# Kernel optimization log

Measured on AMD Instinct MI355X. Metric: run time of the kernel, lower is better.

## Reference

```python
import jax, jax.numpy as jnp
import numpy as np

DX = 1.0
DZ_MIN = 1.0
K = 3  # median filter kernel size (odd)


def median_filter3d(x):
    # x: (N, C, D, H, W); 3x3x3 windowed median with reflect padding.
    p = K // 2
    xp = jnp.pad(x, ((0, 0), (0, 0), (p, p), (p, p), (p, p)), mode='reflect')
    N, C, D, H, W = x.shape
    # 27 shifted views stacked on a new last axis (fixed small loop over kernel offsets)
    wins = jnp.stack(
        [xp[:, :, i:i + D, j:j + H, k:k + W]
         for i in range(K) for j in range(K) for k in range(K)],
        axis=-1,
    )
    # 27 elements (odd) -> torch lower-median == element at index 13 of sorted window
    return jnp.sort(wins, axis=-1)[..., (K * K * K - 1) // 2]


def setup_inputs() -> dict:
    key = jax.random.key(0)
    pred_z = jax.random.normal(key, (1, 1, 128, 192, 193), dtype=jnp.float32)
    return {"pred_z": pred_z, "iepoch": 1, "epoch_max": 100}


def reference(pred_z, iepoch, epoch_max):
    # dz along last (W) axis
    dz = pred_z[..., 1:] - pred_z[..., :-1]
    d = dz / DX
    # windowed-median smoothness loss (no NaNs in inputs -> nanmean == mean)
    smoothz = median_filter3d(d)
    loss_smooth = jnp.mean((d - smoothz) ** 2)
    # monotonicity penalty: max over clamped negative increments
    loss_mon = jnp.max(jnp.maximum(-(dz - DZ_MIN) / DX, 0.0))
    # torch.median over all elements returns sorted[(n-1)//2] (lower median)
    z0 = pred_z[..., 0].reshape(-1)
    n = z0.shape[0]
    loss_average = jnp.sort(z0)[(n - 1) // 2] ** 2
    return (loss_smooth, loss_mon, loss_average)
```

## Files before the change

### kernel.cpp

```cpp
#include <hip/hip_runtime.h>

#define NZ 128
#define NY 192
#define NXP 193
#define NX 192
#define NVOX (NZ * NY * NX)
#define NZ0 (NZ * NY)

#define TX 32
#define TY 16
#define TZ 8
#define LX 34
#define LYP 10
#define LZ 10
#define LSLP (LYP * LX)
#define LTOTP (LZ * LSLP)

#define GX (NX / TX)
#define GY (NY / TY)
#define GZ (NZ / TZ)
#define NBLK (GX * GY * GZ)
#define ZB (NZ0 / 256)

__device__ double   g_ps[NBLK];
__device__ float    g_pm[NBLK];
__device__ unsigned g_hist[2048];
__device__ unsigned g_u[NZ0];

__device__ __forceinline__ int refl(int i, int n) {
    i = (i < 0) ? -i : i;
    i = (i >= n) ? (2 * n - 2 - i) : i;
    return i;
}

__device__ __forceinline__ unsigned f2sortable(float f) {
    unsigned bits = __float_as_uint(f);
    return bits ^ ((bits & 0x80000000u) ? 0xFFFFFFFFu : 0x80000000u);
}

typedef _Float16 H2 __attribute__((ext_vector_type(2)));

static __device__ __forceinline__ H2 h2min(H2 a, H2 b) { return __builtin_elementwise_min(a, b); }
static __device__ __forceinline__ H2 h2max(H2 a, H2 b) { return __builtin_elementwise_max(a, b); }

template<int M, int N>
struct OEM {
    static __device__ __forceinline__ void run(const H2* a, const H2* b, H2* out) {
        if constexpr (M == 0) {
#pragma unroll
            for (int i = 0; i < N; ++i) out[i] = b[i];
        } else if constexpr (N == 0) {
#pragma unroll
            for (int i = 0; i < M; ++i) out[i] = a[i];
        } else if constexpr (M == 1 && N == 1) {
            out[0] = h2min(a[0], b[0]);
            out[1] = h2max(a[0], b[0]);
        } else {
            constexpr int ME = (M + 1) / 2, MO = M / 2, NE = (N + 1) / 2, NO = N / 2;
            H2 ae[ME], be[NE];
            H2 ao[MO > 0 ? MO : 1], bo[NO > 0 ? NO : 1];
#pragma unroll
            for (int i = 0; i < ME; ++i) ae[i] = a[2 * i];
#pragma unroll
            for (int i = 0; i < MO; ++i) ao[i] = a[2 * i + 1];
#pragma unroll
            for (int i = 0; i < NE; ++i) be[i] = b[2 * i];
#pragma unroll
            for (int i = 0; i < NO; ++i) bo[i] = b[2 * i + 1];
            constexpr int EL = ME + NE, OL = MO + NO;
            H2 e[EL];
            H2 o[OL > 0 ? OL : 1];
            OEM<ME, NE>::run(ae, be, e);
            OEM<MO, NO>::run(ao, bo, o);
            constexpr int P = (OL < EL - 1) ? OL : (EL - 1);
            out[0] = e[0];
#pragma unroll
            for (int i = 0; i < P; ++i) {
                out[2 * i + 1] = h2min(o[i], e[i + 1]);
                out[2 * i + 2] = h2max(o[i], e[i + 1]);
            }
            if constexpr (EL == OL)           out[M + N - 1] = o[OL - 1];
            else if constexpr (EL == OL + 2)  out[M + N - 1] = e[EL - 1];
        }
    }
};

template<int N>
struct OES {
    static __device__ __forceinline__ void run(const H2* in, H2* out) {
        if constexpr (N == 1) {
            out[0] = in[0];
        } else {
            constexpr int H = N / 2;
            H2 s1[H], s2[N - H];
            OES<H>::run(in, s1);
            OES<N - H>::run(in + H, s2);
            OEM<H, N - H>::run(s1, s2, out);
        }
    }
};

__device__ __forceinline__ H2 sel27(const H2* A, const H2* M) {
    H2 t0 = h2max(A[0], M[12]);
    H2 t1 = h2max(A[1], M[11]);
    H2 t2 = h2max(A[2], M[10]);
    H2 t3 = h2max(A[3], M[9]);
    H2 t4 = h2max(A[4], M[8]);
    H2 t5 = h2max(A[5], M[7]);
    H2 t6 = h2max(A[6], M[6]);
    H2 t7 = h2max(A[7], M[5]);
    H2 t8 = h2max(A[8], M[4]);
    H2 r0 = h2min(h2min(t0, t1), h2min(t2, t3));
    H2 r1 = h2min(h2min(t4, t5), h2min(t6, t7));
    return h2min(h2min(r0, r1), h2min(t8, M[13]));
}

__global__ __launch_bounds__(256, 4) void fused_main(const float* __restrict__ P) {
    __shared__ H2 dt[LTOTP];
    const int tid = threadIdx.x;
    const int bid = blockIdx.x;

    if (bid < ZB) {
        unsigned* h = (unsigned*)dt;
        for (int j = tid; j < 2048; j += 256) h[j] = 0u;
        __syncthreads();
        const int i = bid * 256 + tid;
        unsigned u = f2sortable(P[(size_t)i * NXP]);
        g_u[i] = u;
        atomicAdd(&h[u >> 21], 1u);
        __syncthreads();
        for (int j = tid; j < 2048; j += 256) {
            unsigned c = h[j];
            if (c) atomicAdd(&g_hist[j], c);
        }
        return;
    }

    const int bf = bid - ZB;
    const int bx = bf % GX;
    const int brem = bf / GX;
    const int by = brem % GY;
    const int bz = brem / GY;
    const int x0 = bx * TX, y0 = by * TY, z0t = bz * TZ;

    int offL[2], offH[2], lp[2];
#pragma unroll
    for (int k = 0; k < 2; ++k) {
        int p = tid + 256 * k;
        lp[k] = (p < LSLP) ? p : -1;
        if (p < LSLP) {
            int xx = p % LX, rr = p / LX;
            int gx  = refl(x0 + xx - 1, NX);
            int gyL = refl(y0 + rr - 1, NY);
            int gyH = refl(y0 + rr + 7, NY);
            offL[k] = gyL * NXP + gx;
            offH[k] = gyH * NXP + gx;
        }
    }
    for (int zz = 0; zz < LZ; ++zz) {
        int gz = refl(z0t + zz - 1, NZ);
        const float* __restrict__ pl = P + (size_t)gz * (NY * NXP);
#pragma unroll
        for (int k = 0; k < 2; ++k) {
            if (lp[k] >= 0) {
                float dL = pl[offL[k] + 1] - pl[offL[k]];
                float dH = pl[offH[k] + 1] - pl[offH[k]];
                H2 v;
                v.x = (_Float16)dL;
                v.y = (_Float16)dH;
                dt[zz * LSLP + lp[k]] = v;
            }
        }
    }
    __syncthreads();

    const int x = tid & 31;
    const int y = tid >> 5;
    const int rbase = y * LX + x;

    auto rd9 = [&](int base, H2* v) {
#pragma unroll
        for (int dy = 0; dy < 3; ++dy)
#pragma unroll
            for (int dxx = 0; dxx < 3; ++dxx)
                v[dy * 3 + dxx] = dt[base + dy * LX + dxx];
    };

    H2 S0[9], S1[9], S2[9], T[9], M[18];
    H2 c2, m2 = (H2)((_Float16)0.0f);
    const H2 one2 = (H2)((_Float16)1.0f);
    float s_acc = 0.0f;

    rd9(rbase, T);            OES<9>::run(T, S0);
    rd9(rbase + LSLP, T);     c2 = T[4];
    OES<9>::run(T, S1);

    auto accum = [&](H2 med) {
        H2 df = c2 - med;
        float dl = (float)df.x, dh = (float)df.y;
        s_acc = fmaf(dl, dl, fmaf(dh, dh, s_acc));
        m2 = h2max(m2, one2 - c2);
    };

    int sl = rbase + 2 * LSLP;
#pragma unroll 1
    for (int t = 0; t < TZ; t += 2) {
        rd9(sl, T);
        H2 cn = T[4];
        OES<9>::run(T, S2);
        OEM<9, 9>::run(S1, S2, M);
        accum(sel27(S0, M));
        c2 = cn;
        sl += LSLP;

        rd9(sl, T);
        cn = T[4];
        OES<9>::run(T, S0);
        accum(sel27(S0, M));
        c2 = cn;
        sl += LSLP;

#pragma unroll
        for (int i = 0; i < 9; ++i) {
            H2 tmp = S0[i];
            S0[i] = S2[i];
            S1[i] = tmp;
        }
    }

    float m_acc = fmaxf((float)m2.x, (float)m2.y);

#pragma unroll
    for (int off = 32; off > 0; off >>= 1) {
        s_acc += __shfl_down(s_acc, off);
        m_acc = fmaxf(m_acc, __shfl_down(m_acc, off));
    }
    __shared__ float ss[4], sm[4];
    const int lane = tid & 63, wid = tid >> 6;
    if (lane == 0) { ss[wid] = s_acc; sm[wid] = m_acc; }
    __syncthreads();
    if (tid == 0) {
        float S = (ss[0] + ss[1]) + (ss[2] + ss[3]);
        float M2 = fmaxf(fmaxf(sm[0], sm[1]), fmaxf(sm[2], sm[3]));
        g_ps[bf] = (double)S;
        g_pm[bf] = M2;
    }
}

__global__ __launch_bounds__(1024) void final_k(float* __restrict__ out) {
    __shared__ unsigned cand[2048];
    __shared__ unsigned s_cnt, s_med, s_b, s_r;
    __shared__ unsigned wsum[16], woff[16];
    const int tid = threadIdx.x;
    const int lane = tid & 63, wid = tid >> 6;
    const unsigned kk = (NZ0 - 1) / 2;

    unsigned h0 = g_hist[2 * tid], h1 = g_hist[2 * tid + 1];
    {
        unsigned mysum = h0 + h1, inc = mysum;
#pragma unroll
        for (int d = 1; d < 64; d <<= 1) { unsigned t2 = __shfl_up(inc, d); if (lane >= d) inc += t2; }
        if (lane == 63) wsum[wid] = inc;
        __syncthreads();
        if (tid == 0) { unsigned a = 0; for (int w = 0; w < 16; ++w) { woff[w] = a; a += wsum[w]; } }
        __syncthreads();
        unsigned exc = woff[wid] + inc - mysum;
        if (exc <= kk && kk < exc + h0) { s_b = 2u * tid; s_r = kk - exc; }
        exc += h0;
        if (exc <= kk && kk < exc + h1) { s_b = 2u * tid + 1u; s_r = kk - exc; }
    }
    __syncthreads();
    const unsigned b1 = s_b, k1 = s_r;
    g_hist[2 * tid] = 0u; g_hist[2 * tid + 1] = 0u;

    if (tid == 0) s_cnt = 0u;
    __syncthreads();
    for (int i = tid; i < NZ0; i += 1024) {
        unsigned u = g_u[i];
        if ((u >> 21) == b1) {
            unsigned idx = atomicAdd(&s_cnt, 1u);
            if (idx < 2048u) cand[idx] = u;
        }
    }
    __syncthreads();
    const unsigned m = s_cnt;

    if (m <= 2048u) {
        for (int i = tid; i < (int)m; i += 1024) {
            unsigned c = cand[i], less = 0u, eq = 0u;
            for (unsigned j = 0; j < m; ++j) {
                unsigned v = cand[j];
                less += (v < c); eq += (v == c);
            }
            if (less <= k1 && k1 < less + eq) s_med = c;
        }
        __syncthreads();
    } else {
        unsigned pref = b1, kx = k1;
        for (int j = tid; j < 2048; j += 1024) cand[j] = 0u;
        __syncthreads();
        for (int i = tid; i < NZ0; i += 1024) {
            unsigned u = g_u[i];
            if ((u >> 21) == pref) atomicAdd(&cand[(u >> 10) & 2047u], 1u);
        }
        __syncthreads();
        {
            unsigned c0 = cand[tid * 2], c1 = cand[tid * 2 + 1];
            unsigned mysum = c0 + c1, inc = mysum;
#pragma unroll
            for (int d = 1; d < 64; d <<= 1) { unsigned t2 = __shfl_up(inc, d); if (lane >= d) inc += t2; }
            if (lane == 63) wsum[wid] = inc;
            __syncthreads();
            if (tid == 0) { unsigned a = 0; for (int w = 0; w < 16; ++w) { woff[w] = a; a += wsum[w]; } }
            __syncthreads();
            unsigned exc = woff[wid] + inc - mysum;
            if (exc <= kx && kx < exc + c0) { s_b = tid * 2u; s_r = kx - exc; }
            exc += c0;
            if (exc <= kx && kx < exc + c1) { s_b = tid * 2u + 1u; s_r = kx - exc; }
        }
        __syncthreads();
        pref = (pref << 11) | s_b; kx = s_r;
        __syncthreads();
        for (int j = tid; j < 1024; j += 1024) cand[j] = 0u;
        __syncthreads();
        for (int i = tid; i < NZ0; i += 1024) {
            unsigned u = g_u[i];
            if ((u >> 10) == pref) atomicAdd(&cand[u & 1023u], 1u);
        }
        __syncthreads();
        {
            unsigned c0 = cand[tid], mysum = c0, inc = mysum;
#pragma unroll
            for (int d = 1; d < 64; d <<= 1) { unsigned t2 = __shfl_up(inc, d); if (lane >= d) inc += t2; }
            if (lane == 63) wsum[wid] = inc;
            __syncthreads();
            if (tid == 0) { unsigned a = 0; for (int w = 0; w < 16; ++w) { woff[w] = a; a += wsum[w]; } }
            __syncthreads();
            unsigned exc = woff[wid] + inc - mysum;
            if (exc <= kx && kx < exc + c0) s_b = (unsigned)tid;
        }
        __syncthreads();
        if (tid == 0) s_med = (pref << 10) | s_b;
        __syncthreads();
    }

    double s = 0.0; float mm = 0.0f;
    for (int i = tid; i < NBLK; i += 1024) {
        s += g_ps[i];
        mm = fmaxf(mm, g_pm[i]);
    }
#pragma unroll
    for (int off = 32; off > 0; off >>= 1) {
        s += __shfl_down(s, off);
        mm = fmaxf(mm, __shfl_down(mm, off));
    }
    __shared__ double sd[16];
    __shared__ float sf[16];
    if (lane == 0) { sd[wid] = s; sf[wid] = mm; }
    __syncthreads();
    if (tid == 0) {
        double S = 0.0; float M = 0.0f;
        for (int w = 0; w < 16; ++w) { S += sd[w]; M = fmaxf(M, sf[w]); }
        unsigned u = s_med;
        unsigned bits = (u & 0x80000000u) ? (u ^ 0x80000000u) : ~u;
        float med = __uint_as_float(bits);
        out[0] = (float)(S / (double)NVOX);
        out[1] = M;
        out[2] = med * med;
    }
}

extern "C" void kernel_launch(void* const* d_in, const int* in_sizes, int n_in,
                              void* d_out, int out_size, void* d_ws, size_t ws_size,
                              hipStream_t stream) {
    const float* P = (const float*)d_in[0];
    float* out = (float*)d_out;

    hipLaunchKernelGGL(fused_main, dim3(ZB + NBLK), dim3(256), 0, stream, P);
    hipLaunchKernelGGL(final_k, dim3(1), dim3(1024), 0, stream, out);
}
```

Before: 95.79 us.

## Fold final reduction into main kernel with last-block and dedicated median block

Removes the second single-block kernel launch. A dedicated block spins until all z0 histogram blocks finish, then runs the radix median selection in parallel with the stencil blocks. The last stencil block, found with an atomic counter, reduces the partial sums and waits on a flag for the median. This saves a launch and the serialized tail, but relies on spin-waiting across blocks (the median block must be co-resident with the histogram blocks) and on global counters being reset correctly.

```diff
diff --git a/kernel.cpp b/kernel.cpp
--- a/kernel.cpp
+++ b/kernel.cpp
@@ -21,11 +21,16 @@
 #define GZ (NZ / TZ)
 #define NBLK (GX * GY * GZ)
 #define ZB (NZ0 / 256)
+#define NGRID (ZB + 1 + NBLK)
 
 __device__ double   g_ps[NBLK];
 __device__ float    g_pm[NBLK];
 __device__ unsigned g_hist[2048];
 __device__ unsigned g_u[NZ0];
+__device__ unsigned g_cnt_g;
+__device__ unsigned g_cnt_t;
+__device__ unsigned g_flag;
+__device__ unsigned g_med;
 
 __device__ __forceinline__ int refl(int i, int n) {
     i = (i < 0) ? -i : i;
@@ -115,7 +120,34 @@
     return h2min(h2min(r0, r1), h2min(t8, M[13]));
 }
 
-__global__ __launch_bounds__(256, 4) void fused_main(const float* __restrict__ P) {
+template<int PER>
+__device__ __forceinline__ void pick256(const unsigned* __restrict__ h, unsigned kk,
+                                        unsigned* s_b, unsigned* s_r,
+                                        unsigned* wsum, unsigned* woff) {
+    const int tid = threadIdx.x;
+    const int lane = tid & 63, wid = tid >> 6;
+    unsigned v[PER];
+    unsigned mysum = 0u;
+#pragma unroll
+    for (int j = 0; j < PER; ++j) { v[j] = h[tid * PER + j]; mysum += v[j]; }
+    unsigned inc = mysum;
+#pragma unroll
+    for (int d = 1; d < 64; d <<= 1) { unsigned t = __shfl_up(inc, d); if (lane >= d) inc += t; }
+    if (lane == 63) wsum[wid] = inc;
+    __syncthreads();
+    if (tid == 0) { unsigned a = 0; for (int w = 0; w < 4; ++w) { woff[w] = a; a += wsum[w]; } }
+    __syncthreads();
+    unsigned exc = woff[wid] + inc - mysum;
+#pragma unroll
+    for (int j = 0; j < PER; ++j) {
+        if (exc <= kk && kk < exc + v[j]) { *s_b = (unsigned)(tid * PER + j); *s_r = kk - exc; }
+        exc += v[j];
+    }
+    __syncthreads();
+}
+
+__global__ __launch_bounds__(256, 4) void fused_main(const float* __restrict__ P,
+                                                     float* __restrict__ out) {
     __shared__ H2 dt[LTOTP];
     const int tid = threadIdx.x;
     const int bid = blockIdx.x;
@@ -133,10 +165,84 @@
             unsigned c = h[j];
             if (c) atomicAdd(&g_hist[j], c);
         }
+        __threadfence();
+        __syncthreads();
+        if (tid == 0) atomicAdd(&g_cnt_g, 1u);
         return;
     }
 
-    const int bf = bid - ZB;
+    if (bid == ZB) {
+        __shared__ unsigned wsum[4], woff[4];
+        __shared__ unsigned s_b, s_r, s_cnt, s_med;
+        unsigned* cand = (unsigned*)dt;
+        const unsigned kk = (NZ0 - 1) / 2;
+
+        if (tid == 0) {
+            while (atomicAdd(&g_cnt_g, 0u) < ZB) __builtin_amdgcn_s_sleep(2);
+        }
+        __syncthreads();
+        __threadfence();
+
+        pick256<8>(g_hist, kk, &s_b, &s_r, wsum, woff);
+        const unsigned b1 = s_b, k1 = s_r;
+        for (int j = tid; j < 2048; j += 256) g_hist[j] = 0u;
+
+        if (tid == 0) s_cnt = 0u;
+        __syncthreads();
+        for (int i = tid; i < NZ0; i += 256) {
+            unsigned u = g_u[i];
+            if ((u >> 21) == b1) {
+                unsigned idx = atomicAdd(&s_cnt, 1u);
+                if (idx < 2048u) cand[idx] = u;
+            }
+        }
+        __syncthreads();
+        const unsigned m = s_cnt;
+
+        if (m <= 2048u) {
+            for (int i = tid; i < (int)m; i += 256) {
+                unsigned c = cand[i], less = 0u, eq = 0u;
+                for (unsigned j = 0; j < m; ++j) {
+                    unsigned v = cand[j];
+                    less += (v < c); eq += (v == c);
+                }
+                if (less <= k1 && k1 < less + eq) s_med = c;
+            }
+            __syncthreads();
+        } else {
+            unsigned pref = b1, kx = k1;
+            for (int j = tid; j < 2048; j += 256) cand[j] = 0u;
+            __syncthreads();
+            for (int i = tid; i < NZ0; i += 256) {
+                unsigned u = g_u[i];
+                if ((u >> 21) == pref) atomicAdd(&cand[(u >> 10) & 2047u], 1u);
+            }
+            __syncthreads();
+            pick256<8>(cand, kx, &s_b, &s_r, wsum, woff);
+            pref = (pref << 11) | s_b; kx = s_r;
+            __syncthreads();
+            for (int j = tid; j < 1024; j += 256) cand[j] = 0u;
+            __syncthreads();
+            for (int i = tid; i < NZ0; i += 256) {
+                unsigned u = g_u[i];
+                if ((u >> 10) == pref) atomicAdd(&cand[u & 1023u], 1u);
+            }
+            __syncthreads();
+            pick256<4>(cand, kx, &s_b, &s_r, wsum, woff);
+            if (tid == 0) s_med = (pref << 10) | s_b;
+            __syncthreads();
+        }
+
+        if (tid == 0) {
+            g_med = s_med;
+            atomicExch(&g_cnt_g, 0u);
+            __threadfence();
+            atomicExch(&g_flag, 1u);
+        }
+        return;
+    }
+
+    const int bf = bid - ZB - 1;
     const int bx = bf % GX;
     const int brem = bf / GX;
     const int by = brem % GY;
@@ -236,6 +342,7 @@
         m_acc = fmaxf(m_acc, __shfl_down(m_acc, off));
     }
     __shared__ float ss[4], sm[4];
+    __shared__ int s_fin;
     const int lane = tid & 63, wid = tid >> 6;
     if (lane == 0) { ss[wid] = s_acc; sm[wid] = m_acc; }
     __syncthreads();
@@ -244,108 +351,16 @@
         float M2 = fmaxf(fmaxf(sm[0], sm[1]), fmaxf(sm[2], sm[3]));
         g_ps[bf] = (double)S;
         g_pm[bf] = M2;
-    }
-}
-
-__global__ __launch_bounds__(1024) void final_k(float* __restrict__ out) {
-    __shared__ unsigned cand[2048];
-    __shared__ unsigned s_cnt, s_med, s_b, s_r;
-    __shared__ unsigned wsum[16], woff[16];
-    const int tid = threadIdx.x;
-    const int lane = tid & 63, wid = tid >> 6;
-    const unsigned kk = (NZ0 - 1) / 2;
-
-    unsigned h0 = g_hist[2 * tid], h1 = g_hist[2 * tid + 1];
-    {
-        unsigned mysum = h0 + h1, inc = mysum;
-#pragma unroll
-        for (int d = 1; d < 64; d <<= 1) { unsigned t2 = __shfl_up(inc, d); if (lane >= d) inc += t2; }
-        if (lane == 63) wsum[wid] = inc;
-        __syncthreads();
-        if (tid == 0) { unsigned a = 0; for (int w = 0; w < 16; ++w) { woff[w] = a; a += wsum[w]; } }
-        __syncthreads();
-        unsigned exc = woff[wid] + inc - mysum;
-        if (exc <= kk && kk < exc + h0) { s_b = 2u * tid; s_r = kk - exc; }
-        exc += h0;
-        if (exc <= kk && kk < exc + h1) { s_b = 2u * tid + 1u; s_r = kk - exc; }
-    }
-    __syncthreads();
-    const unsigned b1 = s_b, k1 = s_r;
-    g_hist[2 * tid] = 0u; g_hist[2 * tid + 1] = 0u;
-
-    if (tid == 0) s_cnt = 0u;
-    __syncthreads();
-    for (int i = tid; i < NZ0; i += 1024) {
-        unsigned u = g_u[i];
-        if ((u >> 21) == b1) {
-            unsigned idx = atomicAdd(&s_cnt, 1u);
-            if (idx < 2048u) cand[idx] = u;
-        }
-    }
-    __syncthreads();
-    const unsigned m = s_cnt;
-
-    if (m <= 2048u) {
-        for (int i = tid; i < (int)m; i += 1024) {
-            unsigned c = cand[i], less = 0u, eq = 0u;
-            for (unsigned j = 0; j < m; ++j) {
-                unsigned v = cand[j];
-                less += (v < c); eq += (v == c);
-            }
-            if (less <= k1 && k1 < less + eq) s_med = c;
-        }
-        __syncthreads();
-    } else {
-        unsigned pref = b1, kx = k1;
-        for (int j = tid; j < 2048; j += 1024) cand[j] = 0u;
-        __syncthreads();
-        for (int i = tid; i < NZ0; i += 1024) {
-            unsigned u = g_u[i];
-            if ((u >> 21) == pref) atomicAdd(&cand[(u >> 10) & 2047u], 1u);
-        }
-        __syncthreads();
-        {
-            unsigned c0 = cand[tid * 2], c1 = cand[tid * 2 + 1];
-            unsigned mysum = c0 + c1, inc = mysum;
-#pragma unroll
-            for (int d = 1; d < 64; d <<= 1) { unsigned t2 = __shfl_up(inc, d); if (lane >= d) inc += t2; }
-            if (lane == 63) wsum[wid] = inc;
-            __syncthreads();
-            if (tid == 0) { unsigned a = 0; for (int w = 0; w < 16; ++w) { woff[w] = a; a += wsum[w]; } }
-            __syncthreads();
-            unsigned exc = woff[wid] + inc - mysum;
-            if (exc <= kx && kx < exc + c0) { s_b = tid * 2u; s_r = kx - exc; }
-            exc += c0;
-            if (exc <= kx && kx < exc + c1) { s_b = tid * 2u + 1u; s_r = kx - exc; }
-        }
-        __syncthreads();
-        pref = (pref << 11) | s_b; kx = s_r;
-        __syncthreads();
-        for (int j = tid; j < 1024; j += 1024) cand[j] = 0u;
-        __syncthreads();
-        for (int i = tid; i < NZ0; i += 1024) {
-            unsigned u = g_u[i];
-            if ((u >> 10) == pref) atomicAdd(&cand[u & 1023u], 1u);
-        }
-        __syncthreads();
-        {
-            unsigned c0 = cand[tid], mysum = c0, inc = mysum;
-#pragma unroll
-            for (int d = 1; d < 64; d <<= 1) { unsigned t2 = __shfl_up(inc, d); if (lane >= d) inc += t2; }
-            if (lane == 63) wsum[wid] = inc;
-            __syncthreads();
-            if (tid == 0) { unsigned a = 0; for (int w = 0; w < 16; ++w) { woff[w] = a; a += wsum[w]; } }
-            __syncthreads();
-            unsigned exc = woff[wid] + inc - mysum;
-            if (exc <= kx && kx < exc + c0) s_b = (unsigned)tid;
-        }
-        __syncthreads();
-        if (tid == 0) s_med = (pref << 10) | s_b;
-        __syncthreads();
-    }
-
+        __threadfence();
+        unsigned old = atomicAdd(&g_cnt_t, 1u);
+        s_fin = (old == NBLK - 1) ? 1 : 0;
+    }
+    __syncthreads();
+    if (!s_fin) return;
+
+    __threadfence();
     double s = 0.0; float mm = 0.0f;
-    for (int i = tid; i < NBLK; i += 1024) {
+    for (int i = tid; i < NBLK; i += 256) {
         s += g_ps[i];
         mm = fmaxf(mm, g_pm[i]);
     }
@@ -354,14 +369,18 @@
         s += __shfl_down(s, off);
         mm = fmaxf(mm, __shfl_down(mm, off));
     }
-    __shared__ double sd[16];
-    __shared__ float sf[16];
+    __shared__ double sd[4];
+    __shared__ float sf[4];
     if (lane == 0) { sd[wid] = s; sf[wid] = mm; }
     __syncthreads();
     if (tid == 0) {
-        double S = 0.0; float M = 0.0f;
-        for (int w = 0; w < 16; ++w) { S += sd[w]; M = fmaxf(M, sf[w]); }
-        unsigned u = s_med;
+        double S = (sd[0] + sd[1]) + (sd[2] + sd[3]);
+        float M = fmaxf(fmaxf(sf[0], sf[1]), fmaxf(sf[2], sf[3]));
+        while (atomicAdd(&g_flag, 0u) == 0u) __builtin_amdgcn_s_sleep(2);
+        __threadfence();
+        unsigned u = g_med;
+        atomicExch(&g_flag, 0u);
+        atomicExch(&g_cnt_t, 0u);
         unsigned bits = (u & 0x80000000u) ? (u ^ 0x80000000u) : ~u;
         float med = __uint_as_float(bits);
         out[0] = (float)(S / (double)NVOX);
@@ -376,6 +395,5 @@
     const float* P = (const float*)d_in[0];
     float* out = (float*)d_out;
 
-    hipLaunchKernelGGL(fused_main, dim3(ZB + NBLK), dim3(256), 0, stream, P);
-    hipLaunchKernelGGL(final_k, dim3(1), dim3(1024), 0, stream, out);
-}
+    hipLaunchKernelGGL(fused_main, dim3(NGRID), dim3(256), 0, stream, P, out);
+}
```

After: 128.5 us. 1.34x slower.
